# Performance work log

Measured on AMD Instinct MI355X. Metric: run time of the kernel, lower is better.

## Reference

```python
import jax, jax.numpy as jnp
import numpy as np

NUM_GROUPS = 40
MAX_DISP = 192 // 4  # 48 disparity planes at 1/4 resolution


def setup_inputs() -> dict:
    key = jax.random.key(0)
    k1, k2, k3, k4 = jax.random.split(key, 4)
    return {
        "left_gwc": jax.random.normal(k1, (4, 320, 64, 128), dtype=jnp.float32),
        "right_gwc": jax.random.normal(k2, (4, 320, 64, 128), dtype=jnp.float32),
        "left_unary": jax.random.normal(k3, (4, 12, 64, 128), dtype=jnp.float32),
        "right_unary": jax.random.normal(k4, (4, 12, 64, 128), dtype=jnp.float32),
    }


def reference(left_gwc, right_gwc, left_unary, right_unary):
    # method='gwc': group-wise correlation cost volume.
    B, C, H, W = left_gwc.shape
    G = NUM_GROUPS
    D = MAX_DISP
    Cg = C // G  # channels per group
    lg = left_gwc.reshape(B, G, Cg, H, W)
    rg = right_gwc.reshape(B, G, Cg, H, W)
    w_idx = jnp.arange(W)  # broadcasts over last (width) axis

    def step(carry, d):
        # shift right features right by d along width; roll wrap is masked below
        r_sh = jnp.roll(rg, d, axis=-1)
        corr = jnp.mean(lg * r_sh, axis=2)  # [B, G, H, W]
        corr = jnp.where(w_idx >= d, corr, jnp.zeros((), corr.dtype))
        return carry, corr

    _, cv = jax.lax.scan(step, None, jnp.arange(D))  # [D, B, G, H, W]
    return jnp.transpose(cv, (1, 2, 0, 3, 4))  # [B, G, D, H, W]
```

## Files before the change

kernel.cpp:

```cpp
#include <hip/hip_runtime.h>


#define NG 40
#define ND 48
#define NCG 8
#define NH 64
#define NW 128

typedef float f32x4 __attribute__((ext_vector_type(4)));

__global__ __launch_bounds__(384) void cost_volume_kernel(
    const float* __restrict__ left, const float* __restrict__ right,
    float* __restrict__ out)
{
    __shared__ float Ls[2][NCG][NW];
    __shared__ float Rs[2][NCG][176];

    const int tid = threadIdx.x;
    const int blk = blockIdx.x;
    const int h2 = blk & 31;
    const int g  = (blk >> 5) % NG;
    const int b  = blk / (NG * 32);

    if (tid < 192) {
        int hr = tid / 96;
        int r  = tid % 96;
        int c  = r / 12;
        int j  = (r % 12) * 4;
        *(float4*)&Rs[hr][c][j] = make_float4(0.f, 0.f, 0.f, 0.f);
    }

    const int h0 = h2 << 1;
    const size_t inbase = (((size_t)b * (NG * NCG) + (size_t)g * NCG) * NH + h0) * NW;
    for (int i = tid; i < 512; i += 384) {
        int c   = i >> 6;
        int rem = i & 63;
        int hr  = rem >> 5;
        int w4  = (rem & 31) << 2;
        const size_t off = inbase + (size_t)c * (NH * NW) + (size_t)rem * 4;
        *(float4*)&Ls[hr][c][w4]      = *(const float4*)&left[off];
        *(float4*)&Rs[hr][c][48 + w4] = *(const float4*)&right[off];
    }
    __syncthreads();

    const int hh = tid / 192;
    const int t  = tid % 192;
    const int wt = t & 31;
    const int dt = t >> 5;
    const int w0 = wt << 2;
    const int d0 = dt << 3;
    const int xa = w0 - d0 + 40;

    float acc[8][4];
#pragma unroll
    for (int d = 0; d < 8; ++d)
#pragma unroll
        for (int w = 0; w < 4; ++w) acc[d][w] = 0.f;

#pragma unroll
    for (int c = 0; c < NCG; ++c) {
        float4 r0 = *(const float4*)&Rs[hh][c][xa];
        float4 r1 = *(const float4*)&Rs[hh][c][xa + 4];
        float4 r2 = *(const float4*)&Rs[hh][c][xa + 8];
        float4 l  = *(const float4*)&Ls[hh][c][w0];
        float rw[12] = {r0.x, r0.y, r0.z, r0.w,
                        r1.x, r1.y, r1.z, r1.w,
                        r2.x, r2.y, r2.z, r2.w};
        float lw[4] = {l.x, l.y, l.z, l.w};
#pragma unroll
        for (int d = 0; d < 8; ++d) {
#pragma unroll
            for (int w = 0; w < 4; ++w) {
                acc[d][w] = fmaf(lw[w], rw[w - d + 8], acc[d][w]);
            }
        }
    }

    const size_t obase = ((((size_t)b * NG + g) * ND + d0) * NH + (h0 + hh)) * NW + w0;
#pragma unroll
    for (int d = 0; d < 8; ++d) {
        f32x4 o;
        o.x = acc[d][0] * 0.125f;
        o.y = acc[d][1] * 0.125f;
        o.z = acc[d][2] * 0.125f;
        o.w = acc[d][3] * 0.125f;
        __builtin_nontemporal_store(o, (f32x4*)&out[obase + (size_t)d * (NH * NW)]);
    }
}

extern "C" void kernel_launch(void* const* d_in, const int* in_sizes, int n_in,
                              void* d_out, int out_size, void* d_ws, size_t ws_size,
                              hipStream_t stream) {
    const float* left  = (const float*)d_in[0];
    const float* right = (const float*)d_in[1];
    float* out = (float*)d_out;
    const int grid = 4 * NG * 32;
    cost_volume_kernel<<<grid, 384, 0, stream>>>(left, right, out);
}
```

Measured before the change: 63.27 us.

## Process four rows per block and loop each thread over two rows

Each block now covers four image rows instead of two, halving the grid. Each wave owns one disparity octet and each thread computes two rows sequentially, reusing its setup. Input loads switch to nontemporal loads. The cost is more shared memory per block and fewer blocks, which may lower occupancy and parallelism for a kernel bound by output writes.

```diff
diff --git a/kernel.cpp b/kernel.cpp
--- a/kernel.cpp
+++ b/kernel.cpp
@@ -13,78 +13,89 @@
     const float* __restrict__ left, const float* __restrict__ right,
     float* __restrict__ out)
 {
-    __shared__ float Ls[2][NCG][NW];
-    __shared__ float Rs[2][NCG][176];
+    __shared__ float Ls[4][NCG][NW];
+    __shared__ float Rs[4][NCG][176];
 
     const int tid = threadIdx.x;
     const int blk = blockIdx.x;
-    const int h2 = blk & 31;
-    const int g  = (blk >> 5) % NG;
-    const int b  = blk / (NG * 32);
+    const int h4 = blk & 15;
+    const int g  = (blk >> 4) % NG;
+    const int b  = blk / (NG * 16);
+    const int h0 = h4 << 2;
 
-    if (tid < 192) {
-        int hr = tid / 96;
-        int r  = tid % 96;
-        int c  = r / 12;
-        int j  = (r % 12) * 4;
-        *(float4*)&Rs[hr][c][j] = make_float4(0.f, 0.f, 0.f, 0.f);
+    {
+        int rc  = tid / 12;
+        int row = rc >> 3;
+        int c   = rc & 7;
+        int j   = (tid % 12) * 4;
+        *(f32x4*)&Rs[row][c][j] = (f32x4)(0.f);
     }
 
-    const int h0 = h2 << 1;
     const size_t inbase = (((size_t)b * (NG * NCG) + (size_t)g * NCG) * NH + h0) * NW;
-    for (int i = tid; i < 512; i += 384) {
-        int c   = i >> 6;
-        int rem = i & 63;
-        int hr  = rem >> 5;
-        int w4  = (rem & 31) << 2;
-        const size_t off = inbase + (size_t)c * (NH * NW) + (size_t)rem * 4;
-        *(float4*)&Ls[hr][c][w4]      = *(const float4*)&left[off];
-        *(float4*)&Rs[hr][c][48 + w4] = *(const float4*)&right[off];
+#pragma unroll
+    for (int ii = 0; ii < 3; ++ii) {
+        int i = tid + ii * 384;
+        if (ii < 2 || i < 1024) {
+            int c   = i >> 7;
+            int rem = i & 127;
+            int row = rem >> 5;
+            int w4  = (rem & 31) << 2;
+            const size_t off = inbase + (size_t)c * (NH * NW) + (size_t)rem * 4;
+            f32x4 lv = __builtin_nontemporal_load((const f32x4*)&left[off]);
+            f32x4 rv = __builtin_nontemporal_load((const f32x4*)&right[off]);
+            *(f32x4*)&Ls[row][c][w4]      = lv;
+            *(f32x4*)&Rs[row][c][48 + w4] = rv;
+        }
     }
     __syncthreads();
 
-    const int hh = tid / 192;
-    const int t  = tid % 192;
-    const int wt = t & 31;
-    const int dt = t >> 5;
-    const int w0 = wt << 2;
-    const int d0 = dt << 3;
-    const int xa = w0 - d0 + 40;
-
-    float acc[8][4];
-#pragma unroll
-    for (int d = 0; d < 8; ++d)
-#pragma unroll
-        for (int w = 0; w < 4; ++w) acc[d][w] = 0.f;
+    const int wave = tid >> 6;
+    const int lane = tid & 63;
+    const int hp   = lane >> 5;
+    const int wt   = lane & 31;
+    const int w0   = wt << 2;
+    const int d0   = wave << 3;
+    const int xa   = w0 - d0 + 40;
 
 #pragma unroll
-    for (int c = 0; c < NCG; ++c) {
-        float4 r0 = *(const float4*)&Rs[hh][c][xa];
-        float4 r1 = *(const float4*)&Rs[hh][c][xa + 4];
-        float4 r2 = *(const float4*)&Rs[hh][c][xa + 8];
-        float4 l  = *(const float4*)&Ls[hh][c][w0];
-        float rw[12] = {r0.x, r0.y, r0.z, r0.w,
-                        r1.x, r1.y, r1.z, r1.w,
-                        r2.x, r2.y, r2.z, r2.w};
-        float lw[4] = {l.x, l.y, l.z, l.w};
+    for (int hpair = 0; hpair < 2; ++hpair) {
+        const int hl = (hpair << 1) + hp;
+
+        float acc[8][4];
+#pragma unroll
+        for (int d = 0; d < 8; ++d)
+#pragma unroll
+            for (int w = 0; w < 4; ++w) acc[d][w] = 0.f;
+
+#pragma unroll
+        for (int c = 0; c < NCG; ++c) {
+            float4 r0 = *(const float4*)&Rs[hl][c][xa];
+            float4 r1 = *(const float4*)&Rs[hl][c][xa + 4];
+            float4 r2 = *(const float4*)&Rs[hl][c][xa + 8];
+            float4 l  = *(const float4*)&Ls[hl][c][w0];
+            float rw[12] = {r0.x, r0.y, r0.z, r0.w,
+                            r1.x, r1.y, r1.z, r1.w,
+                            r2.x, r2.y, r2.z, r2.w};
+            float lw[4] = {l.x, l.y, l.z, l.w};
+#pragma unroll
+            for (int d = 0; d < 8; ++d) {
+#pragma unroll
+                for (int w = 0; w < 4; ++w) {
+                    acc[d][w] = fmaf(lw[w], rw[w - d + 8], acc[d][w]);
+                }
+            }
+        }
+
+        const size_t obase = ((((size_t)b * NG + g) * ND + d0) * NH + (h0 + hl)) * NW + w0;
 #pragma unroll
         for (int d = 0; d < 8; ++d) {
-#pragma unroll
-            for (int w = 0; w < 4; ++w) {
-                acc[d][w] = fmaf(lw[w], rw[w - d + 8], acc[d][w]);
-            }
+            f32x4 o;
+            o.x = acc[d][0] * 0.125f;
+            o.y = acc[d][1] * 0.125f;
+            o.z = acc[d][2] * 0.125f;
+            o.w = acc[d][3] * 0.125f;
+            __builtin_nontemporal_store(o, (f32x4*)&out[obase + (size_t)d * (NH * NW)]);
         }
-    }
-
-    const size_t obase = ((((size_t)b * NG + g) * ND + d0) * NH + (h0 + hh)) * NW + w0;
-#pragma unroll
-    for (int d = 0; d < 8; ++d) {
-        f32x4 o;
-        o.x = acc[d][0] * 0.125f;
-        o.y = acc[d][1] * 0.125f;
-        o.z = acc[d][2] * 0.125f;
-        o.w = acc[d][3] * 0.125f;
-        __builtin_nontemporal_store(o, (f32x4*)&out[obase + (size_t)d * (NH * NW)]);
     }
 }
 
@@ -94,6 +105,6 @@
     const float* left  = (const float*)d_in[0];
     const float* right = (const float*)d_in[1];
     float* out = (float*)d_out;
-    const int grid = 4 * NG * 32;
+    const int grid = 4 * NG * 16;
     cost_volume_kernel<<<grid, 384, 0, stream>>>(left, right, out);
 }
```

Measured after the change: 66.35 us. 1.05x slower.

## Process four row-pairs per block with register-prefetched right rows and direct left loads

Applied to the files above, without the earlier changes.

Each block now covers eight rows (four iterations of two rows) instead of two, cutting the grid by four. Right-feature rows for the next iteration are prefetched into registers with nontemporal loads while the current iteration computes, then written to a single shared buffer between barriers. Left features are read straight from global memory instead of being staged in shared memory. The aim is to hide load latency and cut per-block overhead, at the cost of fewer blocks in flight, two barriers per iteration, and uncached global loads of left data in the inner loop.

```diff
diff --git a/kernel.cpp b/kernel.cpp
--- a/kernel.cpp
+++ b/kernel.cpp
@@ -13,78 +13,95 @@
     const float* __restrict__ left, const float* __restrict__ right,
     float* __restrict__ out)
 {
-    __shared__ float Ls[2][NCG][NW];
     __shared__ float Rs[2][NCG][176];
 
     const int tid = threadIdx.x;
     const int blk = blockIdx.x;
-    const int h2 = blk & 31;
-    const int g  = (blk >> 5) % NG;
-    const int b  = blk / (NG * 32);
+    const int oct = blk & 7;
+    const int g   = (blk >> 3) % NG;
+    const int b   = blk / (NG * 8);
+    const int h0  = oct << 3;
 
     if (tid < 192) {
         int hr = tid / 96;
         int r  = tid % 96;
         int c  = r / 12;
         int j  = (r % 12) * 4;
-        *(float4*)&Rs[hr][c][j] = make_float4(0.f, 0.f, 0.f, 0.f);
+        *(f32x4*)&Rs[hr][c][j] = (f32x4)(0.f);
     }
 
-    const int h0 = h2 << 1;
-    const size_t inbase = (((size_t)b * (NG * NCG) + (size_t)g * NCG) * NH + h0) * NW;
-    for (int i = tid; i < 512; i += 384) {
-        int c   = i >> 6;
-        int rem = i & 63;
-        int hr  = rem >> 5;
-        int w4  = (rem & 31) << 2;
-        const size_t off = inbase + (size_t)c * (NH * NW) + (size_t)rem * 4;
-        *(float4*)&Ls[hr][c][w4]      = *(const float4*)&left[off];
-        *(float4*)&Rs[hr][c][48 + w4] = *(const float4*)&right[off];
-    }
-    __syncthreads();
+    const int  i0   = tid;
+    const int  c0   = i0 >> 6, rem0 = i0 & 63;
+    const int  hr0  = rem0 >> 5, w40 = (rem0 & 31) << 2;
+    const int  i1   = tid + 384;
+    const int  c1   = i1 >> 6, rem1 = i1 & 63;
+    const int  hr1  = rem1 >> 5, w41 = (rem1 & 31) << 2;
+    const bool has1 = (tid < 128);
+
+    const size_t base = ((size_t)b * 320 + (size_t)g * NCG) * (size_t)(NH * NW);
+    const size_t roff0 = base + (size_t)c0 * (NH * NW) + (size_t)(h0 + hr0) * NW + w40;
+    const size_t roff1 = base + (size_t)c1 * (NH * NW) + (size_t)(h0 + hr1) * NW + w41;
 
     const int hh = tid / 192;
     const int t  = tid % 192;
     const int wt = t & 31;
-    const int dt = t >> 5;
+    const int dt = t / 32;
     const int w0 = wt << 2;
     const int d0 = dt << 3;
     const int xa = w0 - d0 + 40;
 
-    float acc[8][4];
+    f32x4 v0 = __builtin_nontemporal_load((const f32x4*)&right[roff0]);
+    f32x4 v1;
+    if (has1) v1 = __builtin_nontemporal_load((const f32x4*)&right[roff1]);
+
+    for (int s = 0; s < 4; ++s) {
+        __syncthreads();
+        *(f32x4*)&Rs[hr0][c0][48 + w40] = v0;
+        if (has1) *(f32x4*)&Rs[hr1][c1][48 + w41] = v1;
+        if (s < 3) {
+            const size_t d = (size_t)(2 * (s + 1)) * NW;
+            v0 = __builtin_nontemporal_load((const f32x4*)&right[roff0 + d]);
+            if (has1) v1 = __builtin_nontemporal_load((const f32x4*)&right[roff1 + d]);
+        }
+        __syncthreads();
+
+        const int h = h0 + 2 * s + hh;
+
+        float acc[8][4];
 #pragma unroll
-    for (int d = 0; d < 8; ++d)
+        for (int d = 0; d < 8; ++d)
 #pragma unroll
-        for (int w = 0; w < 4; ++w) acc[d][w] = 0.f;
+            for (int w = 0; w < 4; ++w) acc[d][w] = 0.f;
 
 #pragma unroll
-    for (int c = 0; c < NCG; ++c) {
-        float4 r0 = *(const float4*)&Rs[hh][c][xa];
-        float4 r1 = *(const float4*)&Rs[hh][c][xa + 4];
-        float4 r2 = *(const float4*)&Rs[hh][c][xa + 8];
-        float4 l  = *(const float4*)&Ls[hh][c][w0];
-        float rw[12] = {r0.x, r0.y, r0.z, r0.w,
-                        r1.x, r1.y, r1.z, r1.w,
-                        r2.x, r2.y, r2.z, r2.w};
-        float lw[4] = {l.x, l.y, l.z, l.w};
+        for (int c = 0; c < NCG; ++c) {
+            float4 l  = *(const float4*)&left[base + (size_t)c * (NH * NW) + (size_t)h * NW + w0];
+            float4 r0 = *(const float4*)&Rs[hh][c][xa];
+            float4 r1 = *(const float4*)&Rs[hh][c][xa + 4];
+            float4 r2 = *(const float4*)&Rs[hh][c][xa + 8];
+            float rw[12] = {r0.x, r0.y, r0.z, r0.w,
+                            r1.x, r1.y, r1.z, r1.w,
+                            r2.x, r2.y, r2.z, r2.w};
+            float lw[4] = {l.x, l.y, l.z, l.w};
+#pragma unroll
+            for (int d = 0; d < 8; ++d) {
+#pragma unroll
+                for (int w = 0; w < 4; ++w) {
+                    acc[d][w] = fmaf(lw[w], rw[w - d + 8], acc[d][w]);
+                }
+            }
+        }
+
+        const size_t obase = ((((size_t)b * NG + g) * ND + d0) * NH + h) * NW + w0;
 #pragma unroll
         for (int d = 0; d < 8; ++d) {
-#pragma unroll
-            for (int w = 0; w < 4; ++w) {
-                acc[d][w] = fmaf(lw[w], rw[w - d + 8], acc[d][w]);
-            }
+            f32x4 o;
+            o.x = acc[d][0] * 0.125f;
+            o.y = acc[d][1] * 0.125f;
+            o.z = acc[d][2] * 0.125f;
+            o.w = acc[d][3] * 0.125f;
+            __builtin_nontemporal_store(o, (f32x4*)&out[obase + (size_t)d * (NH * NW)]);
         }
-    }
-
-    const size_t obase = ((((size_t)b * NG + g) * ND + d0) * NH + (h0 + hh)) * NW + w0;
-#pragma unroll
-    for (int d = 0; d < 8; ++d) {
-        f32x4 o;
-        o.x = acc[d][0] * 0.125f;
-        o.y = acc[d][1] * 0.125f;
-        o.z = acc[d][2] * 0.125f;
-        o.w = acc[d][3] * 0.125f;
-        __builtin_nontemporal_store(o, (f32x4*)&out[obase + (size_t)d * (NH * NW)]);
     }
 }
 
@@ -94,6 +111,6 @@
     const float* left  = (const float*)d_in[0];
     const float* right = (const float*)d_in[1];
     float* out = (float*)d_out;
-    const int grid = 4 * NG * 32;
+    const int grid = 4 * NG * 8;
     cost_volume_kernel<<<grid, 384, 0, stream>>>(left, right, out);
 }
```

Result: no change. 63.50 us (+0.4%).
